# Kernel tuning notes

Measured on AMD Instinct MI355X. Metric: run time of the kernel, lower is better.

Reference implementation:

```python
import jax, jax.numpy as jnp
import numpy as np

B, S, D = 4, 2048, 1024
H = 16
HD = D // H  # 64


def setup_inputs() -> dict:
    key = jax.random.key(0)
    ks = jax.random.split(key, 8)
    scale = 1.0 / np.sqrt(D)
    return {
        "hidden_states": jax.random.normal(ks[0], (B, S, D), dtype=jnp.float32),
        "attention_mask": jnp.ones((B, 1, 1, S), dtype=jnp.int32),
        "Wq": jax.random.normal(ks[1], (D, D), dtype=jnp.float32) * scale,
        "bq": jax.random.normal(ks[2], (D,), dtype=jnp.float32) * 0.02,
        "Wk": jax.random.normal(ks[3], (D, D), dtype=jnp.float32) * scale,
        "bk": jax.random.normal(ks[4], (D,), dtype=jnp.float32) * 0.02,
        "Wv": jax.random.normal(ks[5], (D, D), dtype=jnp.float32) * scale,
        "bv": jax.random.normal(ks[6], (D,), dtype=jnp.float32) * 0.02,
    }


def _split_heads(x):
    # [b, t, (h d)] -> [b, h, t, d]
    b, t, _ = x.shape
    return x.reshape(b, t, H, HD).transpose(0, 2, 1, 3)


def reference(hidden_states, attention_mask, Wq, bq, Wk, bk, Wv, bv):
    # Linear projections (torch Linear: x @ W.T + b)
    q = _split_heads(hidden_states @ Wq.T + bq)
    k = _split_heads(hidden_states @ Wk.T + bk)
    v = _split_heads(hidden_states @ Wv.T + bv)

    # scaled dot-product scores: [b, h, s, s]
    scores = jnp.einsum("bhqd,bhkd->bhqk", q, k) / np.sqrt(HD)

    s = scores.shape[-1]
    causal = jnp.tril(jnp.ones((s, s), dtype=bool))[None, None]
    neg_inf = jnp.float32(-jnp.inf)
    scores = jnp.where(causal, scores, neg_inf)
    # attention_mask is 0/1 keep mask: [b, 1, 1, s]
    scores = jnp.where(attention_mask == 0, neg_inf, scores)

    probs = jax.nn.softmax(scores, axis=-1)  # dropout p=0 (eval)
    ctx = jnp.einsum("bhqk,bhkd->bhqd", probs, v)
    # [b, h, t, d] -> [b, t, h*d]
    return ctx.transpose(0, 2, 1, 3).reshape(hidden_states.shape[0], s, D)
```

## Files before the change

kernel.cpp:

```cpp
#include <hip/hip_runtime.h>
#include <hip/hip_bf16.h>
#include <math.h>


#define B_ 4
#define S_ 2048
#define D_ 1024
#define H_ 16
#define HD_ 64
#define M_ (B_ * S_)

typedef unsigned short u16;
typedef unsigned int u32;
typedef __attribute__((ext_vector_type(4))) float f32x4;
typedef __attribute__((ext_vector_type(8))) short bf16x8;

__device__ __forceinline__ u16 f2bfu_rn(float x) {
    u32 u = __builtin_bit_cast(u32, x);
    return (u16)((u + 0x8000u) >> 16);
}

__device__ __forceinline__ void gl2lds16(const void* g, void* l) {
    __builtin_amdgcn_global_load_lds(
        (const __attribute__((address_space(1))) u32*)g,
        (__attribute__((address_space(3))) u32*)l, 16, 0, 0);
}

#define XN  8388608u
#define WN  1048576u
__global__ __launch_bounds__(256) void convert_bf16(
    const float* __restrict__ X,  const float* __restrict__ Wq,
    const float* __restrict__ Wk, const float* __restrict__ Wv,
    u16* __restrict__ Xb, u16* __restrict__ Wqb,
    u16* __restrict__ Wkb, u16* __restrict__ Wvb)
{
    size_t idx = ((size_t)blockIdx.x * 256 + threadIdx.x) * 8;
    const float* src; u16* dst; size_t off;
    if (idx < XN)                { src = X;  dst = Xb;  off = idx; }
    else if (idx < XN + WN)      { src = Wq; dst = Wqb; off = idx - XN; }
    else if (idx < XN + 2 * WN)  { src = Wk; dst = Wkb; off = idx - XN - WN; }
    else                         { src = Wv; dst = Wvb; off = idx - XN - 2 * WN; }
    float4 a = *(const float4*)(src + off);
    float4 b = *(const float4*)(src + off + 4);
    uint4 o;
    o.x = (u32)f2bfu_rn(a.x) | ((u32)f2bfu_rn(a.y) << 16);
    o.y = (u32)f2bfu_rn(a.z) | ((u32)f2bfu_rn(a.w) << 16);
    o.z = (u32)f2bfu_rn(b.x) | ((u32)f2bfu_rn(b.y) << 16);
    o.w = (u32)f2bfu_rn(b.z) | ((u32)f2bfu_rn(b.w) << 16);
    *(uint4*)(dst + off) = o;
}

#define QSCALE 0.18033688011112042f

__global__ __launch_bounds__(512) void qkv_mfma8(
    const u16* __restrict__ Xb,
    const u16* __restrict__ Wqb, const u16* __restrict__ Wkb,
    const u16* __restrict__ Wvb,
    const float* __restrict__ bq, const float* __restrict__ bk,
    const float* __restrict__ bv,
    u16* __restrict__ Qb, u16* __restrict__ Kb, u16* __restrict__ Vtb)
{
    const int which = blockIdx.y;
    const int bxl = ((blockIdx.x & 7) << 5) | (blockIdx.x >> 3);

    const u16* Asrc; const u16* Bsrc; const float* bias; u16* Out;
    int m0, n0;
    if (which == 0)      { Asrc = Xb;  Bsrc = Wqb; bias = bq; Out = Qb;
                           m0 = (bxl >> 2) * 128; n0 = (bxl & 3) * 256; }
    else if (which == 1) { Asrc = Xb;  Bsrc = Wkb; bias = bk; Out = Kb;
                           m0 = (bxl >> 2) * 128; n0 = (bxl & 3) * 256; }
    else                 { Asrc = Wvb; Bsrc = Xb;  bias = bv; Out = Vtb;
                           m0 = (bxl >> 5) * 128; n0 = (bxl & 31) * 256; }

    __shared__ u16 As[3][128][64];
    __shared__ u16 Bs[3][256][64];

    const int t = threadIdx.x;
    const int wave = t >> 6, lane = t & 63;
    const int qd = lane >> 4, l15 = lane & 15;
    const int wm = wave >> 2, wn = wave & 3;

    auto STAGE_A = [&](int tt, int u) {
        const int buf = tt % 3, k0 = tt * 64;
        const int rb = u * 64 + wave * 8;
        const int r  = rb + (lane >> 3);
        const int g  = (lane & 7) ^ (r & 7);
        gl2lds16(Asrc + (size_t)(m0 + r) * D_ + k0 + g * 8, &As[buf][rb][0]);
    };
    auto STAGE_B = [&](int tt, int q) {
        const int buf = tt % 3, k0 = tt * 64;
        const int rb = q * 64 + wave * 8;
        const int r  = rb + (lane >> 3);
        const int g  = (lane & 7) ^ (r & 7);
        gl2lds16(Bsrc + (size_t)(n0 + r) * D_ + k0 + g * 8, &Bs[buf][rb][0]);
    };

    const f32x4 zero = {0.f, 0.f, 0.f, 0.f};
    f32x4 acc[4][4];
#pragma unroll
    for (int i = 0; i < 4; ++i)
#pragma unroll
        for (int j = 0; j < 4; ++j) acc[i][j] = zero;

#pragma unroll
    for (int u = 0; u < 2; ++u) STAGE_A(0, u);
#pragma unroll
    for (int q = 0; q < 4; ++q) STAGE_B(0, q);
#pragma unroll
    for (int u = 0; u < 2; ++u) STAGE_A(1, u);
#pragma unroll
    for (int q = 0; q < 4; ++q) STAGE_B(1, q);
    asm volatile("s_waitcnt vmcnt(6)" ::: "memory");
    __builtin_amdgcn_s_barrier();

    for (int tt = 0; tt < 16; ++tt) {
        const int buf = tt % 3;
        const bool st = tt < 14;
        const int t2 = tt + 2;

        bf16x8 bfv[4][2];
        bf16x8 af[2];

#pragma unroll
        for (int nt = 0; nt < 4; ++nt) {
            const int row = wn * 64 + nt * 16 + l15;
#pragma unroll
            for (int ks = 0; ks < 2; ++ks)
                bfv[nt][ks] = *(const bf16x8*)&Bs[buf][row][((ks * 4 + qd) ^ (row & 7)) * 8];
        }
        {
            const int row = wm * 64 + l15;
#pragma unroll
            for (int ks = 0; ks < 2; ++ks)
                af[ks] = *(const bf16x8*)&As[buf][row][((ks * 4 + qd) ^ (row & 7)) * 8];
        }
        if (st) { STAGE_A(t2, 0); STAGE_A(t2, 1); }
        __builtin_amdgcn_s_barrier();
        asm volatile("s_waitcnt lgkmcnt(0)" ::: "memory");
        __builtin_amdgcn_sched_barrier(0);
        __builtin_amdgcn_s_setprio(1);
#pragma unroll
        for (int ks = 0; ks < 2; ++ks)
#pragma unroll
            for (int nt = 0; nt < 4; ++nt)
                acc[0][nt] = __builtin_amdgcn_mfma_f32_16x16x32_bf16(
                    af[ks], bfv[nt][ks], acc[0][nt], 0, 0, 0);
        __builtin_amdgcn_s_setprio(0);
        __builtin_amdgcn_s_barrier();

#pragma unroll
        for (int mt = 1; mt < 4; ++mt) {
            const int row = wm * 64 + mt * 16 + l15;
#pragma unroll
            for (int ks = 0; ks < 2; ++ks)
                af[ks] = *(const bf16x8*)&As[buf][row][((ks * 4 + qd) ^ (row & 7)) * 8];
            if (st) {
                if (mt == 1)      { STAGE_B(t2, 0); STAGE_B(t2, 1); }
                else if (mt == 2) { STAGE_B(t2, 2); }
                else              { STAGE_B(t2, 3); }
            }
            __builtin_amdgcn_s_barrier();
            asm volatile("s_waitcnt lgkmcnt(0)" ::: "memory");
            __builtin_amdgcn_sched_barrier(0);
            __builtin_amdgcn_s_setprio(1);
#pragma unroll
            for (int ks = 0; ks < 2; ++ks)
#pragma unroll
                for (int nt = 0; nt < 4; ++nt)
                    acc[mt][nt] = __builtin_amdgcn_mfma_f32_16x16x32_bf16(
                        af[ks], bfv[nt][ks], acc[mt][nt], 0, 0, 0);
            __builtin_amdgcn_s_setprio(0);
            if (mt == 3) {
                if (st) asm volatile("s_waitcnt vmcnt(6)" ::: "memory");
                else    asm volatile("s_waitcnt vmcnt(0)" ::: "memory");
            }
            __builtin_amdgcn_s_barrier();
        }
    }

    if (which < 2) {
#pragma unroll
        for (int nt = 0; nt < 4; ++nt) {
            int n = n0 + wn * 64 + nt * 16 + l15;
            float bv_ = bias[n];
            int h = n >> 6, hd = n & 63;
#pragma unroll
            for (int mt = 0; mt < 4; ++mt)
#pragma unroll
                for (int r = 0; r < 4; ++r) {
                    int m = m0 + wm * 64 + mt * 16 + qd * 4 + r;
                    int bb = m >> 11, s = m & 2047;
                    float v = acc[mt][nt][r] + bv_;
                    if (which == 0) v *= QSCALE;
                    Out[(((size_t)(bb * H_ + h)) * S_ + s) * HD_ + hd] = f2bfu_rn(v);
                }
        }
    } else {
#pragma unroll
        for (int mt = 0; mt < 4; ++mt)
#pragma unroll
            for (int r = 0; r < 4; ++r) {
                int f = m0 + wm * 64 + mt * 16 + qd * 4 + r;
                float bv_ = bias[f];
                int h = f >> 6, hd = f & 63;
#pragma unroll
                for (int nt = 0; nt < 4; ++nt) {
                    int tok = n0 + wn * 64 + nt * 16 + l15;
                    int bb = tok >> 11, s = tok & 2047;
                    float v = acc[mt][nt][r] + bv_;
                    Out[(((size_t)(bb * H_ + h)) * HD_ + hd) * S_ + s] = f2bfu_rn(v);
                }
            }
    }
}

__global__ __launch_bounds__(256) void attn_chunk(
    const u16* __restrict__ Qb, const u16* __restrict__ Kb,
    const u16* __restrict__ Vtb, const int* __restrict__ amask,
    float* __restrict__ Oout, float* __restrict__ Opart,
    float* __restrict__ L0, float* __restrict__ L1)
{
    const int x = blockIdx.x;
    const int bh = blockIdx.y;
    const int b = bh >> 4, h = bh & 15;
    int qt, jt0, jt1; bool second;
    if (x < 32) { qt = 31 - x; jt0 = 0;  jt1 = min(qt, 15); second = false; }
    else        { qt = 63 - x; jt0 = 16; jt1 = qt;          second = true;  }
    const int q0 = qt * 64;

    const int t = threadIdx.x;
    const int wave = t >> 6, lane = t & 63;
    const int qd = lane >> 4, l15 = lane & 15;

    __shared__ u16 Ks[64][64];
    __shared__ u16 Vts[64][64];
    __shared__ u16 Ps[64][72];
    __shared__ float mb[64];

    const size_t base = (size_t)bh * S_ * HD_;
    const u16* Qg = Qb + base;
    const u16* Kg = Kb + base;
    const u16* Vg = Vtb + base;
    const int* am = amask + b * S_;

    bf16x8 qf[2];
    {
        const u16* qrow = Qg + (size_t)(q0 + wave * 16 + l15) * HD_;
        qf[0] = *(const bf16x8*)(qrow + qd * 8);
        qf[1] = *(const bf16x8*)(qrow + 32 + qd * 8);
    }
    bf16x8 onesf;
    {
        short v = (l15 == 0) ? (short)0x3F80 : (short)0;
        onesf = (bf16x8){v, v, v, v, v, v, v, v};
    }

    const f32x4 zero = {0.f, 0.f, 0.f, 0.f};
    f32x4 o[5];
#pragma unroll
    for (int i = 0; i < 5; ++i) o[i] = zero;

    for (int jt = jt0; jt <= jt1; ++jt) {
        const int j0 = jt * 64;
        __syncthreads();
#pragma unroll
        for (int i = 0; i < 2; ++i) {
            int r0  = (wave * 2 + i) * 8;
            int row = r0 + (lane >> 3);
            int g   = (lane & 7) ^ (row & 7);
            gl2lds16(Kg + (size_t)(j0 + row) * HD_ + g * 8, &Ks[r0][0]);
            gl2lds16(Vg + (size_t)row * S_ + j0 + g * 8, &Vts[r0][0]);
        }
        if (t < 64) mb[t] = (am[j0 + t] == 0) ? -1e30f : 0.0f;
        __syncthreads();

        f32x4 sacc[4];
#pragma unroll
        for (int nt = 0; nt < 4; ++nt) sacc[nt] = zero;
#pragma unroll
        for (int ks = 0; ks < 2; ++ks) {
#pragma unroll
            for (int nt = 0; nt < 4; ++nt) {
                int brow = nt * 16 + l15;
                int bp = (ks * 4 + qd) ^ (brow & 7);
                bf16x8 bf = *(const bf16x8*)&Ks[brow][bp * 8];
                sacc[nt] = __builtin_amdgcn_mfma_f32_16x16x32_bf16(
                    qf[ks], bf, sacc[nt], 0, 0, 0);
            }
        }

        float bias[4];
#pragma unroll
        for (int nt = 0; nt < 4; ++nt) bias[nt] = mb[nt * 16 + l15];
        const bool diag = (jt == qt);
#pragma unroll
        for (int r = 0; r < 4; ++r) {
            int prow = wave * 16 + qd * 4 + r;
#pragma unroll
            for (int nt = 0; nt < 4; ++nt) {
                int col = nt * 16 + l15;
                float s = sacc[nt][r] + bias[nt];
                if (diag && col > prow) s = -1e30f;
                float p = __builtin_amdgcn_exp2f(s);
                Ps[prow][col] = f2bfu_rn(p);
            }
        }

#pragma unroll
        for (int ks = 0; ks < 2; ++ks) {
            int arow = wave * 16 + l15;
            bf16x8 pf = *(const bf16x8*)&Ps[arow][ks * 32 + qd * 8];
#pragma unroll
            for (int nt = 0; nt < 4; ++nt) {
                int brow = nt * 16 + l15;
                int bp = (ks * 4 + qd) ^ (brow & 7);
                bf16x8 vf = *(const bf16x8*)&Vts[brow][bp * 8];
                o[nt] = __builtin_amdgcn_mfma_f32_16x16x32_bf16(
                    pf, vf, o[nt], 0, 0, 0);
            }
            o[4] = __builtin_amdgcn_mfma_f32_16x16x32_bf16(
                pf, onesf, o[4], 0, 0, 0);
        }
    }

    if (!second) {
        if (qt <= 15) {
#pragma unroll
            for (int r = 0; r < 4; ++r) {
                float l = __shfl(o[4][r], lane & 48);
                float inv = 1.0f / l;
                int q = q0 + wave * 16 + qd * 4 + r;
                float* op = Oout + ((size_t)(b * S_ + q)) * D_ + h * HD_;
#pragma unroll
                for (int nt = 0; nt < 4; ++nt)
                    op[nt * 16 + l15] = o[nt][r] * inv;
            }
        } else {
#pragma unroll
            for (int r = 0; r < 4; ++r) {
                int q = q0 + wave * 16 + qd * 4 + r;
                float* op = Oout + ((size_t)(b * S_ + q)) * D_ + h * HD_;
#pragma unroll
                for (int nt = 0; nt < 4; ++nt)
                    op[nt * 16 + l15] = o[nt][r];
                if (l15 == 0) L0[(size_t)bh * S_ + q] = o[4][r];
            }
        }
    } else {
#pragma unroll
        for (int r = 0; r < 4; ++r) {
            int q = q0 + wave * 16 + qd * 4 + r;
            int sh = q - 1024;
            float* op = Opart + ((size_t)bh * 1024 + sh) * HD_;
#pragma unroll
            for (int nt = 0; nt < 4; ++nt)
                op[nt * 16 + l15] = o[nt][r];
            if (l15 == 0) L1[(size_t)bh * 1024 + sh] = o[4][r];
        }
    }
}

__global__ __launch_bounds__(256) void combine(
    float* __restrict__ out, const float* __restrict__ Opart,
    const float* __restrict__ L0, const float* __restrict__ L1)
{
    size_t i = ((size_t)blockIdx.x * 256 + threadIdx.x) * 4;
    int d  = (int)(i & (D_ - 1));
    int bs = (int)(i >> 10);
    int b  = bs >> 10, sh = bs & 1023;
    int s  = sh + 1024;
    int h  = d >> 6;
    int bh = b * H_ + h;
    float l = L0[(size_t)bh * S_ + s] + L1[(size_t)bh * 1024 + sh];
    float inv = 1.0f / l;
    float* op = out + ((size_t)(b * S_ + s)) * D_ + d;
    const float* pp = Opart + ((size_t)bh * 1024 + sh) * HD_ + (d & 63);
    float4 v = *(float4*)op;
    float4 p = *(const float4*)pp;
    v.x = (v.x + p.x) * inv; v.y = (v.y + p.y) * inv;
    v.z = (v.z + p.z) * inv; v.w = (v.w + p.w) * inv;
    *(float4*)op = v;
}

extern "C" void kernel_launch(void* const* d_in, const int* in_sizes, int n_in,
                              void* d_out, int out_size, void* d_ws, size_t ws_size,
                              hipStream_t stream) {
    (void)in_sizes; (void)n_in; (void)out_size; (void)ws_size;
    const float* X    = (const float*)d_in[0];
    const int*   mask = (const int*)d_in[1];
    const float* Wq   = (const float*)d_in[2];
    const float* bq   = (const float*)d_in[3];
    const float* Wk   = (const float*)d_in[4];
    const float* bk   = (const float*)d_in[5];
    const float* Wv   = (const float*)d_in[6];
    const float* bv   = (const float*)d_in[7];
    float* out = (float*)d_out;

    u16* Xb  = (u16*)d_ws;
    u16* Wqb = Xb  + XN;
    u16* Wkb = Wqb + WN;
    u16* Wvb = Wkb + WN;
    u16* Qb  = Wvb + WN;
    u16* Kb  = Qb  + XN;
    u16* Vtb = Kb  + XN;
    float* Opart = (float*)(Vtb + XN);
    float* L0 = Opart + (size_t)64 * 1024 * 64;
    float* L1 = L0 + (size_t)64 * 2048;

    convert_bf16<<<(XN + 3 * WN) / (256 * 8), 256, 0, stream>>>(
        X, Wq, Wk, Wv, Xb, Wqb, Wkb, Wvb);
    qkv_mfma8<<<dim3(256, 3), 512, 0, stream>>>(
        Xb, Wqb, Wkb, Wvb, bq, bk, bv, Qb, Kb, Vtb);
    attn_chunk<<<dim3(48, B_ * H_), 256, 0, stream>>>(
        Qb, Kb, Vtb, mask, out, Opart, L0, L1);
    combine<<<(B_ * 1024 * D_ / 4) / 256, 256, 0, stream>>>(out, Opart, L0, L1);
}
```

Before: 263.4 us.

## Prefetch next K/V tile into registers and overlap with MFMA compute

```diff
diff --git a/kernel.cpp b/kernel.cpp
--- a/kernel.cpp
+++ b/kernel.cpp
@@ -231,11 +231,12 @@
     const int t = threadIdx.x;
     const int wave = t >> 6, lane = t & 63;
     const int qd = lane >> 4, l15 = lane & 15;
+    const int srow = (lane >> 3) & 7;
+    const int scol = lane & 7;
 
     __shared__ u16 Ks[64][64];
     __shared__ u16 Vts[64][64];
     __shared__ u16 Ps[64][72];
-    __shared__ float mb[64];
 
     const size_t base = (size_t)bh * S_ * HD_;
     const u16* Qg = Qb + base;
@@ -260,23 +261,47 @@
 #pragma unroll
     for (int i = 0; i < 5; ++i) o[i] = zero;
 
+    bf16x8 kreg[2], vreg[2];
+    int areg[4];
+
+    auto LOADKV = [&](int jt) {
+        const int j0 = jt * 64;
+#pragma unroll
+        for (int i = 0; i < 2; ++i) {
+            int row = (wave * 2 + i) * 8 + srow;
+            int g   = scol ^ srow;
+            kreg[i] = *(const bf16x8*)(Kg + (size_t)(j0 + row) * HD_ + g * 8);
+            vreg[i] = *(const bf16x8*)(Vg + (size_t)row * S_ + j0 + g * 8);
+        }
+#pragma unroll
+        for (int nt = 0; nt < 4; ++nt)
+            areg[nt] = am[j0 + nt * 16 + l15];
+    };
+    auto WRITEKV = [&]() {
+#pragma unroll
+        for (int i = 0; i < 2; ++i) {
+            int r = (wave * 2 + i) * 8 + srow;
+            *(bf16x8*)&Ks[r][scol * 8]  = kreg[i];
+            *(bf16x8*)&Vts[r][scol * 8] = vreg[i];
+        }
+    };
+
+    LOADKV(jt0);
+    WRITEKV();
+    __syncthreads();
+
     for (int jt = jt0; jt <= jt1; ++jt) {
-        const int j0 = jt * 64;
-        __syncthreads();
-#pragma unroll
-        for (int i = 0; i < 2; ++i) {
-            int r0  = (wave * 2 + i) * 8;
-            int row = r0 + (lane >> 3);
-            int g   = (lane & 7) ^ (row & 7);
-            gl2lds16(Kg + (size_t)(j0 + row) * HD_ + g * 8, &Ks[r0][0]);
-            gl2lds16(Vg + (size_t)row * S_ + j0 + g * 8, &Vts[r0][0]);
-        }
-        if (t < 64) mb[t] = (am[j0 + t] == 0) ? -1e30f : 0.0f;
-        __syncthreads();
+        float bias[4];
+#pragma unroll
+        for (int nt = 0; nt < 4; ++nt)
+            bias[nt] = (areg[nt] == 0) ? -1e30f : 0.0f;
+
+        if (jt < jt1) LOADKV(jt + 1);
 
         f32x4 sacc[4];
 #pragma unroll
         for (int nt = 0; nt < 4; ++nt) sacc[nt] = zero;
+        __builtin_amdgcn_s_setprio(1);
 #pragma unroll
         for (int ks = 0; ks < 2; ++ks) {
 #pragma unroll
@@ -288,10 +313,8 @@
                     qf[ks], bf, sacc[nt], 0, 0, 0);
             }
         }
-
-        float bias[4];
-#pragma unroll
-        for (int nt = 0; nt < 4; ++nt) bias[nt] = mb[nt * 16 + l15];
+        __builtin_amdgcn_s_setprio(0);
+
         const bool diag = (jt == qt);
 #pragma unroll
         for (int r = 0; r < 4; ++r) {
@@ -306,6 +329,7 @@
             }
         }
 
+        __builtin_amdgcn_s_setprio(1);
 #pragma unroll
         for (int ks = 0; ks < 2; ++ks) {
             int arow = wave * 16 + l15;
@@ -320,6 +344,13 @@
             }
             o[4] = __builtin_amdgcn_mfma_f32_16x16x32_bf16(
                 pf, onesf, o[4], 0, 0, 0);
+        }
+        __builtin_amdgcn_s_setprio(0);
+
+        if (jt < jt1) {
+            __syncthreads();
+            WRITEKV();
+            __syncthreads();
         }
     }
 
```

New measurement: 273.6 us. 1.04x slower.

## Transpose QK^T MFMA to write P rows vectorized, add setprio and swizzled grid

Applied to the files above, without the earlier changes.

```diff
diff --git a/kernel.cpp b/kernel.cpp
--- a/kernel.cpp
+++ b/kernel.cpp
@@ -220,8 +220,9 @@
     float* __restrict__ Oout, float* __restrict__ Opart,
     float* __restrict__ L0, float* __restrict__ L1)
 {
-    const int x = blockIdx.x;
-    const int bh = blockIdx.y;
+    const int bid = blockIdx.x;
+    const int x   = bid >> 6;
+    const int bh  = ((bid & 7) << 3) | ((bid >> 3) & 7);
     const int b = bh >> 4, h = bh & 15;
     int qt, jt0, jt1; bool second;
     if (x < 32) { qt = 31 - x; jt0 = 0;  jt1 = min(qt, 15); second = false; }
@@ -259,6 +260,9 @@
     f32x4 o[5];
 #pragma unroll
     for (int i = 0; i < 5; ++i) o[i] = zero;
+
+    const int qloc = wave * 16 + l15;
+    u32* prow32 = (u32*)&Ps[qloc][0];
 
     for (int jt = jt0; jt <= jt1; ++jt) {
         const int j0 = jt * 64;
@@ -277,35 +281,39 @@
         f32x4 sacc[4];
 #pragma unroll
         for (int nt = 0; nt < 4; ++nt) sacc[nt] = zero;
+        __builtin_amdgcn_s_setprio(1);
 #pragma unroll
         for (int ks = 0; ks < 2; ++ks) {
 #pragma unroll
             for (int nt = 0; nt < 4; ++nt) {
-                int brow = nt * 16 + l15;
-                int bp = (ks * 4 + qd) ^ (brow & 7);
-                bf16x8 bf = *(const bf16x8*)&Ks[brow][bp * 8];
+                int arow = nt * 16 + l15;
+                int ap = (ks * 4 + qd) ^ (arow & 7);
+                bf16x8 kf = *(const bf16x8*)&Ks[arow][ap * 8];
                 sacc[nt] = __builtin_amdgcn_mfma_f32_16x16x32_bf16(
-                    qf[ks], bf, sacc[nt], 0, 0, 0);
-            }
-        }
-
-        float bias[4];
-#pragma unroll
-        for (int nt = 0; nt < 4; ++nt) bias[nt] = mb[nt * 16 + l15];
+                    kf, qf[ks], sacc[nt], 0, 0, 0);
+            }
+        }
+        __builtin_amdgcn_s_setprio(0);
+
         const bool diag = (jt == qt);
 #pragma unroll
-        for (int r = 0; r < 4; ++r) {
-            int prow = wave * 16 + qd * 4 + r;
-#pragma unroll
-            for (int nt = 0; nt < 4; ++nt) {
-                int col = nt * 16 + l15;
-                float s = sacc[nt][r] + bias[nt];
-                if (diag && col > prow) s = -1e30f;
-                float p = __builtin_amdgcn_exp2f(s);
-                Ps[prow][col] = f2bfu_rn(p);
-            }
-        }
-
+        for (int nt = 0; nt < 4; ++nt) {
+            float4 m4 = *(const float4*)&mb[nt * 16 + qd * 4];
+            float p[4];
+#pragma unroll
+            for (int r = 0; r < 4; ++r) {
+                int kl = nt * 16 + qd * 4 + r;
+                float s = sacc[nt][r] + ((const float*)&m4)[r];
+                if (diag && kl > qloc) s = -1e30f;
+                p[r] = __builtin_amdgcn_exp2f(s);
+            }
+            uint2 w;
+            w.x = (u32)f2bfu_rn(p[0]) | ((u32)f2bfu_rn(p[1]) << 16);
+            w.y = (u32)f2bfu_rn(p[2]) | ((u32)f2bfu_rn(p[3]) << 16);
+            *(uint2*)&prow32[nt * 8 + qd * 2] = w;
+        }
+
+        __builtin_amdgcn_s_setprio(1);
 #pragma unroll
         for (int ks = 0; ks < 2; ++ks) {
             int arow = wave * 16 + l15;
@@ -321,6 +329,7 @@
             o[4] = __builtin_amdgcn_mfma_f32_16x16x32_bf16(
                 pf, onesf, o[4], 0, 0, 0);
         }
+        __builtin_amdgcn_s_setprio(0);
     }
 
     if (!second) {
@@ -411,7 +420,7 @@
         X, Wq, Wk, Wv, Xb, Wqb, Wkb, Wvb);
     qkv_mfma8<<<dim3(256, 3), 512, 0, stream>>>(
         Xb, Wqb, Wkb, Wvb, bq, bk, bv, Qb, Kb, Vtb);
-    attn_chunk<<<dim3(48, B_ * H_), 256, 0, stream>>>(
+    attn_chunk<<<dim3(3072), 256, 0, stream>>>(
         Qb, Kb, Vtb, mask, out, Opart, L0, L1);
     combine<<<(B_ * 1024 * D_ / 4) / 256, 256, 0, stream>>>(out, Opart, L0, L1);
 }
```

After: 243.8 us. -7.4%, faster.
